# Performance work log

Measured on AMD Instinct MI355X. Metric: run time of the kernel, lower is better.

Reference implementation:

```python
import jax, jax.numpy as jnp
import numpy as np

N_GRID = 262144   # grid vertices (all local, empty halo)
N_MESH = 40962    # icosahedral mesh level-6 vertices
N_EDGES = 524288  # mesh2grid bipartite edges
H = 128           # cfg.model.hidden_dim
LN_EPS = 1e-5


def layer_norm(x, g, b):
    m = jnp.mean(x, axis=-1, keepdims=True)
    v = jnp.var(x, axis=-1, keepdims=True)
    return (x - m) * jax.lax.rsqrt(v + LN_EPS) * g + b


def setup_inputs() -> dict:
    key = jax.random.key(0)
    ks = jax.random.split(key, 12)
    def w(k, shape, fan_in):
        return jax.random.normal(k, shape, jnp.float32) * (fan_in ** -0.5)
    return {
        "mesh2grid_edge_features": jax.random.normal(ks[0], (N_EDGES, H), jnp.float32),
        "grid_node_features": jax.random.normal(ks[1], (N_GRID, H), jnp.float32),
        "mesh_node_features": jax.random.normal(ks[2], (N_MESH, H), jnp.float32),
        # edge MLP: Linear(3H->H) -> SiLU -> Linear(H->H) -> LayerNorm, residual
        "edge_W1": w(ks[3], (3 * H, H), 3 * H), "edge_b1": jnp.zeros((H,), jnp.float32),
        "edge_W2": w(ks[4], (H, H), H), "edge_b2": jnp.zeros((H,), jnp.float32),
        "edge_ln_g": jnp.ones((H,), jnp.float32), "edge_ln_b": jnp.zeros((H,), jnp.float32),
        # node MLP: Linear(2H->H) -> SiLU -> Linear(H->H) -> LayerNorm
        "node_W1": w(ks[5], (2 * H, H), 2 * H), "node_b1": jnp.zeros((H,), jnp.float32),
        "node_W2": w(ks[6], (H, H), H), "node_b2": jnp.zeros((H,), jnp.float32),
        "node_ln_g": jnp.ones((H,), jnp.float32), "node_ln_b": jnp.zeros((H,), jnp.float32),
        "src_indices": jax.random.randint(ks[7], (N_EDGES,), 0, N_MESH, jnp.int32),
        "dst_indices": jax.random.randint(ks[8], (N_EDGES,), 0, N_GRID, jnp.int32),
    }


def reference(mesh2grid_edge_features, grid_node_features, mesh_node_features,
              edge_W1, edge_b1, edge_W2, edge_b2, edge_ln_g, edge_ln_b,
              node_W1, node_b1, node_W2, node_b2, node_ln_g, node_ln_b,
              src_indices, dst_indices):
    # --- edge block: gather src (mesh) / dst (grid), MLP, LN, residual ---
    src = mesh_node_features[src_indices]        # [E, H]  (augmented mesh == mesh, empty halo)
    dst = grid_node_features[dst_indices]        # [E, H]
    xe = jnp.concatenate([src, dst, mesh2grid_edge_features], axis=-1)  # [E, 3H]
    he = (jax.nn.silu(xe @ edge_W1 + edge_b1)) @ edge_W2 + edge_b2
    e_feats = mesh2grid_edge_features + layer_norm(he, edge_ln_g, edge_ln_b)  # [E, H]
    # --- node block: scatter-sum edges to grid nodes, MLP, LN ---
    agg = jax.ops.segment_sum(e_feats, dst_indices, num_segments=N_GRID)  # [N_grid, H]
    xn = jnp.concatenate([grid_node_features, agg], axis=-1)              # [N_grid, 2H]
    hn = (jax.nn.silu(xn @ node_W1 + node_b1)) @ node_W2 + node_b2
    n_feats = layer_norm(hn, node_ln_g, node_ln_b)
    return grid_node_features + n_feats
```

## Files before the change

### kernel.cpp

```cpp
#include <hip/hip_runtime.h>
#include <stdint.h>

#define HDIM 128
#define NGRID 262144
#define NMESH 40962
#define NEDGE 524288

typedef __attribute__((ext_vector_type(8))) short short8;
typedef __attribute__((ext_vector_type(4))) float f32x4;

__device__ __forceinline__ unsigned short f2bf(float f) {
  union { float f; uint32_t u; } v; v.f = f;
  uint32_t u = v.u;
  u += 0x7fffu + ((u >> 16) & 1u);
  return (unsigned short)(u >> 16);
}
__device__ __forceinline__ float bf2f(unsigned short h) {
  union { uint32_t u; float f; } v; v.u = ((uint32_t)h) << 16;
  return v.f;
}
__device__ __forceinline__ short8 cvt8(float4 a, float4 b) {
  short8 r;
  r[0] = (short)f2bf(a.x); r[1] = (short)f2bf(a.y);
  r[2] = (short)f2bf(a.z); r[3] = (short)f2bf(a.w);
  r[4] = (short)f2bf(b.x); r[5] = (short)f2bf(b.y);
  r[6] = (short)f2bf(b.z); r[7] = (short)f2bf(b.w);
  return r;
}

__global__ void pack_weights(const float* __restrict__ eW1, const float* __restrict__ eW2,
                             const float* __restrict__ nW1, const float* __restrict__ nW2,
                             unsigned short* __restrict__ ws)
{
  int i = blockIdx.x * 256 + threadIdx.x;
  unsigned short* eW1T = ws;
  unsigned short* eW2T = ws + 49152;
  unsigned short* nW1T = ws + 65536;
  unsigned short* nW2T = ws + 98304;
  if (i < 49152) {
    int c = i / 384, k = i % 384;
    eW1T[i] = f2bf(eW1[(size_t)k * 128 + c]);
  } else if (i < 65536) {
    int j = i - 49152; int c = j / 128, k = j % 128;
    eW2T[j] = f2bf(eW2[(size_t)k * 128 + c]);
  } else if (i < 98304) {
    int j = i - 65536; int c = j / 256, k = j % 256;
    nW1T[j] = f2bf(nW1[(size_t)k * 128 + c]);
  } else if (i < 114688) {
    int j = i - 98304; int c = j / 128, k = j % 128;
    nW2T[j] = f2bf(nW2[(size_t)k * 128 + c]);
  }
}

__global__ __launch_bounds__(256, 4)
void edge_kernel(const float* __restrict__ ef, const float* __restrict__ gridf,
                 const float* __restrict__ mesh,
                 const unsigned short* __restrict__ W1T, const unsigned short* __restrict__ W2T,
                 const float* __restrict__ b1, const float* __restrict__ b2,
                 const float* __restrict__ lng, const float* __restrict__ lnb,
                 const int* __restrict__ src, const int* __restrict__ dst,
                 float* __restrict__ agg)
{
  __shared__ __align__(16) unsigned short h1s[64][136];

  const int tid  = threadIdx.x;
  const int wave = tid >> 6;
  const int lane = tid & 63;
  const int l16  = lane & 15;
  const int g4   = lane >> 4;
  const int e0   = blockIdx.x * 64;
  const int arow = wave * 16 + l16;

  const int myS = src[e0 + arow];
  const int myD = dst[e0 + arow];
  const float* rowS = mesh  + (size_t)myS * HDIM;
  const float* rowD = gridf + (size_t)myD * HDIM;
  const float* rowE = ef    + (size_t)(e0 + arow) * HDIM;

  f32x4 acc[8];
  #pragma unroll
  for (int c = 0; c < 8; ++c) acc[c] = (f32x4){0.f, 0.f, 0.f, 0.f};

  const unsigned short* wl1 = W1T + (size_t)l16 * 384 + g4 * 8;

  #pragma unroll
  for (int part = 0; part < 3; ++part) {
    const float* base = (part == 0) ? rowS : (part == 1) ? rowD : rowE;
    #pragma unroll
    for (int kk = 0; kk < 4; ++kk) {
      const int ks = part * 4 + kk;
      const float* ap = base + kk * 32 + g4 * 8;
      float4 f0 = *reinterpret_cast<const float4*>(ap);
      float4 f1 = *reinterpret_cast<const float4*>(ap + 4);
      short8 a = cvt8(f0, f1);
      #pragma unroll
      for (int c = 0; c < 8; ++c) {
        short8 b = *reinterpret_cast<const short8*>(wl1 + (size_t)c * 16 * 384 + ks * 32);
        acc[c] = __builtin_amdgcn_mfma_f32_16x16x32_bf16(a, b, acc[c], 0, 0, 0);
      }
    }
  }

  #pragma unroll
  for (int c = 0; c < 8; ++c) {
    const int col = c * 16 + l16;
    float bb = b1[col];
    #pragma unroll
    for (int r = 0; r < 4; ++r) {
      float x = acc[c][r] + bb;
      float s = x / (1.f + __expf(-x));
      unsigned int h = f2bf(s);
      unsigned int other = __shfl_xor((int)h, 1);
      unsigned int packed = (l16 & 1) ? ((h << 16) | other) : ((other << 16) | h);
      if ((l16 & 1) == (r & 1)) {
        *reinterpret_cast<unsigned int*>(&h1s[wave * 16 + g4 * 4 + r][c * 16 + (l16 & ~1)]) = packed;
      }
    }
  }
  __syncthreads();

  f32x4 acc2[8];
  #pragma unroll
  for (int c = 0; c < 8; ++c) acc2[c] = (f32x4){0.f, 0.f, 0.f, 0.f};

  const unsigned short* wl2 = W2T + (size_t)l16 * 128 + g4 * 8;
  #pragma unroll
  for (int ks = 0; ks < 4; ++ks) {
    short8 a = *reinterpret_cast<const short8*>(&h1s[arow][ks * 32 + g4 * 8]);
    #pragma unroll
    for (int c = 0; c < 8; ++c) {
      short8 b = *reinterpret_cast<const short8*>(wl2 + (size_t)c * 16 * 128 + ks * 32);
      acc2[c] = __builtin_amdgcn_mfma_f32_16x16x32_bf16(a, b, acc2[c], 0, 0, 0);
    }
  }

  float vs[4] = {0.f, 0.f, 0.f, 0.f};
  float vq[4] = {0.f, 0.f, 0.f, 0.f};
  #pragma unroll
  for (int c = 0; c < 8; ++c) {
    float bb = b2[c * 16 + l16];
    #pragma unroll
    for (int r = 0; r < 4; ++r) {
      float x = acc2[c][r] + bb;
      acc2[c][r] = x;
      vs[r] += x;
      vq[r] += x * x;
    }
  }
  #pragma unroll
  for (int m = 1; m < 16; m <<= 1) {
    #pragma unroll
    for (int r = 0; r < 4; ++r) {
      vs[r] += __shfl_xor(vs[r], m);
      vq[r] += __shfl_xor(vq[r], m);
    }
  }
  float mean[4], rstd[4];
  #pragma unroll
  for (int r = 0; r < 4; ++r) {
    mean[r] = vs[r] * (1.f / 128.f);
    float var = vq[r] * (1.f / 128.f) - mean[r] * mean[r];
    rstd[r] = rsqrtf(var + 1e-5f);
  }
  int drow[4];
  #pragma unroll
  for (int r = 0; r < 4; ++r) drow[r] = dst[e0 + wave * 16 + g4 * 4 + r];

  #pragma unroll
  for (int c = 0; c < 8; ++c) {
    const int col = c * 16 + l16;
    float gg = lng[col], bb = lnb[col];
    #pragma unroll
    for (int r = 0; r < 4; ++r) {
      const int row = wave * 16 + g4 * 4 + r;
      float y = (acc2[c][r] - mean[r]) * rstd[r] * gg + bb;
      float e = ef[(size_t)(e0 + row) * HDIM + col] + y;
      unsafeAtomicAdd(&agg[(size_t)drow[r] * HDIM + col], e);
    }
  }
}

__global__ __launch_bounds__(256, 4)
void node_kernel(const float* __restrict__ gridf,
                 const unsigned short* __restrict__ W1T, const unsigned short* __restrict__ W2T,
                 const float* __restrict__ b1, const float* __restrict__ b2,
                 const float* __restrict__ lng, const float* __restrict__ lnb,
                 float* __restrict__ out)
{
  __shared__ __align__(16) unsigned short h1s[64][136];

  const int tid  = threadIdx.x;
  const int wave = tid >> 6;
  const int lane = tid & 63;
  const int l16  = lane & 15;
  const int g4   = lane >> 4;
  const int n0   = blockIdx.x * 64;
  const int arow = wave * 16 + l16;

  const float* rowG = gridf + (size_t)(n0 + arow) * HDIM;
  const float* rowA = out   + (size_t)(n0 + arow) * HDIM;

  f32x4 acc[8];
  #pragma unroll
  for (int c = 0; c < 8; ++c) acc[c] = (f32x4){0.f, 0.f, 0.f, 0.f};

  const unsigned short* wl1 = W1T + (size_t)l16 * 256 + g4 * 8;

  #pragma unroll
  for (int part = 0; part < 2; ++part) {
    const float* base = (part == 0) ? rowG : rowA;
    #pragma unroll
    for (int kk = 0; kk < 4; ++kk) {
      const int ks = part * 4 + kk;
      const float* ap = base + kk * 32 + g4 * 8;
      float4 f0 = *reinterpret_cast<const float4*>(ap);
      float4 f1 = *reinterpret_cast<const float4*>(ap + 4);
      short8 a = cvt8(f0, f1);
      #pragma unroll
      for (int c = 0; c < 8; ++c) {
        short8 b = *reinterpret_cast<const short8*>(wl1 + (size_t)c * 16 * 256 + ks * 32);
        acc[c] = __builtin_amdgcn_mfma_f32_16x16x32_bf16(a, b, acc[c], 0, 0, 0);
      }
    }
  }

  #pragma unroll
  for (int c = 0; c < 8; ++c) {
    const int col = c * 16 + l16;
    float bb = b1[col];
    #pragma unroll
    for (int r = 0; r < 4; ++r) {
      float x = acc[c][r] + bb;
      float s = x / (1.f + __expf(-x));
      unsigned int h = f2bf(s);
      unsigned int other = __shfl_xor((int)h, 1);
      unsigned int packed = (l16 & 1) ? ((h << 16) | other) : ((other << 16) | h);
      if ((l16 & 1) == (r & 1)) {
        *reinterpret_cast<unsigned int*>(&h1s[wave * 16 + g4 * 4 + r][c * 16 + (l16 & ~1)]) = packed;
      }
    }
  }
  __syncthreads();

  f32x4 acc2[8];
  #pragma unroll
  for (int c = 0; c < 8; ++c) acc2[c] = (f32x4){0.f, 0.f, 0.f, 0.f};

  const unsigned short* wl2 = W2T + (size_t)l16 * 128 + g4 * 8;
  #pragma unroll
  for (int ks = 0; ks < 4; ++ks) {
    short8 a = *reinterpret_cast<const short8*>(&h1s[arow][ks * 32 + g4 * 8]);
    #pragma unroll
    for (int c = 0; c < 8; ++c) {
      short8 b = *reinterpret_cast<const short8*>(wl2 + (size_t)c * 16 * 128 + ks * 32);
      acc2[c] = __builtin_amdgcn_mfma_f32_16x16x32_bf16(a, b, acc2[c], 0, 0, 0);
    }
  }

  float vs[4] = {0.f, 0.f, 0.f, 0.f};
  float vq[4] = {0.f, 0.f, 0.f, 0.f};
  #pragma unroll
  for (int c = 0; c < 8; ++c) {
    float bb = b2[c * 16 + l16];
    #pragma unroll
    for (int r = 0; r < 4; ++r) {
      float x = acc2[c][r] + bb;
      acc2[c][r] = x;
      vs[r] += x;
      vq[r] += x * x;
    }
  }
  #pragma unroll
  for (int m = 1; m < 16; m <<= 1) {
    #pragma unroll
    for (int r = 0; r < 4; ++r) {
      vs[r] += __shfl_xor(vs[r], m);
      vq[r] += __shfl_xor(vq[r], m);
    }
  }
  float mean[4], rstd[4];
  #pragma unroll
  for (int r = 0; r < 4; ++r) {
    mean[r] = vs[r] * (1.f / 128.f);
    float var = vq[r] * (1.f / 128.f) - mean[r] * mean[r];
    rstd[r] = rsqrtf(var + 1e-5f);
  }
  #pragma unroll
  for (int c = 0; c < 8; ++c) {
    const int col = c * 16 + l16;
    float gg = lng[col], bb = lnb[col];
    #pragma unroll
    for (int r = 0; r < 4; ++r) {
      const int row = wave * 16 + g4 * 4 + r;
      size_t idx = (size_t)(n0 + row) * HDIM + col;
      float y = (acc2[c][r] - mean[r]) * rstd[r] * gg + bb;
      out[idx] = gridf[idx] + y;
    }
  }
}

extern "C" void kernel_launch(void* const* d_in, const int* in_sizes, int n_in,
                              void* d_out, int out_size, void* d_ws, size_t ws_size,
                              hipStream_t stream)
{
  (void)in_sizes; (void)n_in; (void)out_size; (void)ws_size;
  const float* ef   = (const float*)d_in[0];
  const float* grid = (const float*)d_in[1];
  const float* mesh = (const float*)d_in[2];
  const float* eW1  = (const float*)d_in[3];
  const float* eb1  = (const float*)d_in[4];
  const float* eW2  = (const float*)d_in[5];
  const float* eb2  = (const float*)d_in[6];
  const float* elng = (const float*)d_in[7];
  const float* elnb = (const float*)d_in[8];
  const float* nW1  = (const float*)d_in[9];
  const float* nb1  = (const float*)d_in[10];
  const float* nW2  = (const float*)d_in[11];
  const float* nb2  = (const float*)d_in[12];
  const float* nlng = (const float*)d_in[13];
  const float* nlnb = (const float*)d_in[14];
  const int* src    = (const int*)d_in[15];
  const int* dst    = (const int*)d_in[16];
  float* out = (float*)d_out;
  unsigned short* ws = (unsigned short*)d_ws;

  hipMemsetAsync(out, 0, (size_t)NGRID * HDIM * sizeof(float), stream);
  pack_weights<<<448, 256, 0, stream>>>(eW1, eW2, nW1, nW2, ws);
  edge_kernel<<<NEDGE / 64, 256, 0, stream>>>(ef, grid, mesh,
      ws, ws + 49152, eb1, eb2, elng, elnb, src, dst, out);
  node_kernel<<<NGRID / 64, 256, 0, stream>>>(grid,
      ws + 65536, ws + 98304, nb1, nb2, nlng, nlnb, out);
}
```

Measured before the change: 957.4 us.

## Sort edges by destination and replace atomic scatter with CSR segmented reduce

Adds a counting sort of edges by destination: histogram, three-pass scan and scatter, with packed src/dst/edge ids. When the workspace is large enough, the edge kernel processes edges in sorted order and writes per-edge bf16 results. The node kernel then sums each grid node's contiguous edge range through row pointers, which removes the float atomics and the output memset. The change also drops the block barrier between the two matmuls, since each wave reads back only its own rows. In exchange it adds several preprocessing launches, a large bf16 intermediate buffer and some precision loss from storing edge outputs in bf16.

```diff
diff --git a/kernel.cpp b/kernel.cpp
--- a/kernel.cpp
+++ b/kernel.cpp
@@ -8,96 +8,158 @@
 
 typedef __attribute__((ext_vector_type(8))) short short8;
 typedef __attribute__((ext_vector_type(4))) float f32x4;
-
-__device__ __forceinline__ unsigned short f2bf(float f) {
-  union { float f; uint32_t u; } v; v.f = f;
-  uint32_t u = v.u;
+typedef unsigned int u32;
+typedef unsigned long long u64;
+
+#define WS_COUNT   0x000000u
+#define WS_ROWPTR  0x100000u
+#define WS_WLOC    0x200010u
+#define WS_BSUM    0x300100u
+#define WS_SORTED  0x310000u
+#define WS_WEIGHTS 0x800000u
+#define WS_ESORT   0x840000u
+#define WE1 0u
+#define WE2 49152u
+#define WN1 65536u
+#define WN2 98304u
+
+static __device__ __forceinline__ u32 f2bf_u(float f) {
+  union { float f; u32 u; } v; v.f = f;
+  u32 u = v.u;
   u += 0x7fffu + ((u >> 16) & 1u);
-  return (unsigned short)(u >> 16);
-}
-__device__ __forceinline__ float bf2f(unsigned short h) {
-  union { uint32_t u; float f; } v; v.u = ((uint32_t)h) << 16;
+  return u >> 16;
+}
+static __device__ __forceinline__ unsigned short f2bf(float f) { return (unsigned short)f2bf_u(f); }
+static __device__ __forceinline__ float bf2f(unsigned short h) {
+  union { u32 u; float f; } v; v.u = ((u32)h) << 16;
   return v.f;
 }
-__device__ __forceinline__ short8 cvt8(float4 a, float4 b) {
+static __device__ __forceinline__ short8 cvt8(const float* p) {
+  float4 f0 = *(const float4*)p;
+  float4 f1 = *(const float4*)(p + 4);
   short8 r;
-  r[0] = (short)f2bf(a.x); r[1] = (short)f2bf(a.y);
-  r[2] = (short)f2bf(a.z); r[3] = (short)f2bf(a.w);
-  r[4] = (short)f2bf(b.x); r[5] = (short)f2bf(b.y);
-  r[6] = (short)f2bf(b.z); r[7] = (short)f2bf(b.w);
+  r[0] = (short)f2bf_u(f0.x); r[1] = (short)f2bf_u(f0.y);
+  r[2] = (short)f2bf_u(f0.z); r[3] = (short)f2bf_u(f0.w);
+  r[4] = (short)f2bf_u(f1.x); r[5] = (short)f2bf_u(f1.y);
+  r[6] = (short)f2bf_u(f1.z); r[7] = (short)f2bf_u(f1.w);
   return r;
 }
 
 __global__ void pack_weights(const float* __restrict__ eW1, const float* __restrict__ eW2,
                              const float* __restrict__ nW1, const float* __restrict__ nW2,
-                             unsigned short* __restrict__ ws)
+                             unsigned short* __restrict__ wp)
 {
   int i = blockIdx.x * 256 + threadIdx.x;
-  unsigned short* eW1T = ws;
-  unsigned short* eW2T = ws + 49152;
-  unsigned short* nW1T = ws + 65536;
-  unsigned short* nW2T = ws + 98304;
   if (i < 49152) {
     int c = i / 384, k = i % 384;
-    eW1T[i] = f2bf(eW1[(size_t)k * 128 + c]);
+    wp[WE1 + i] = f2bf(eW1[(size_t)k * 128 + c]);
   } else if (i < 65536) {
     int j = i - 49152; int c = j / 128, k = j % 128;
-    eW2T[j] = f2bf(eW2[(size_t)k * 128 + c]);
+    wp[WE2 + j] = f2bf(eW2[(size_t)k * 128 + c]);
   } else if (i < 98304) {
     int j = i - 65536; int c = j / 256, k = j % 256;
-    nW1T[j] = f2bf(nW1[(size_t)k * 128 + c]);
+    wp[WN1 + j] = f2bf(nW1[(size_t)k * 128 + c]);
   } else if (i < 114688) {
     int j = i - 98304; int c = j / 128, k = j % 128;
-    nW2T[j] = f2bf(nW2[(size_t)k * 128 + c]);
-  }
-}
-
+    wp[WN2 + j] = f2bf(nW2[(size_t)k * 128 + c]);
+  }
+}
+
+__global__ void hist_k(const int* __restrict__ dst, u32* __restrict__ cnt) {
+  int e = blockIdx.x * 256 + threadIdx.x;
+  atomicAdd(&cnt[dst[e]], 1u);
+}
+
+__global__ void scan1(const u32* __restrict__ cnt, u32* __restrict__ rp, u32* __restrict__ bsum) {
+  int t = threadIdx.x, b = blockIdx.x;
+  int i0 = b * 1024 + t * 4;
+  uint4 v = *(const uint4*)(cnt + i0);
+  u32 s = v.x + v.y + v.z + v.w;
+  u32 sc = s;
+  #pragma unroll
+  for (int d = 1; d < 64; d <<= 1) {
+    u32 n = (u32)__shfl_up((int)sc, d);
+    if ((t & 63) >= d) sc += n;
+  }
+  __shared__ u32 wsum[4];
+  if ((t & 63) == 63) wsum[t >> 6] = sc;
+  __syncthreads();
+  u32 woff = 0;
+  for (int w = 0; w < (t >> 6); ++w) woff += wsum[w];
+  u32 ex = woff + sc - s;
+  rp[i0] = ex; rp[i0 + 1] = ex + v.x; rp[i0 + 2] = ex + v.x + v.y; rp[i0 + 3] = ex + v.x + v.y + v.z;
+  if (t == 255) bsum[b] = woff + sc;
+}
+
+__global__ void scan2(u32* __restrict__ bsum) {
+  int t = threadIdx.x;
+  u32 s = bsum[t];
+  u32 sc = s;
+  #pragma unroll
+  for (int d = 1; d < 64; d <<= 1) {
+    u32 n = (u32)__shfl_up((int)sc, d);
+    if ((t & 63) >= d) sc += n;
+  }
+  __shared__ u32 wsum[4];
+  if ((t & 63) == 63) wsum[t >> 6] = sc;
+  __syncthreads();
+  u32 woff = 0;
+  for (int w = 0; w < (t >> 6); ++w) woff += wsum[w];
+  bsum[t] = woff + sc - s;
+}
+
+__global__ void scan3(u32* __restrict__ rp, u32* __restrict__ wloc, const u32* __restrict__ bsum) {
+  int t = threadIdx.x, b = blockIdx.x;
+  int i0 = b * 1024 + t * 4;
+  u32 off = bsum[b];
+  #pragma unroll
+  for (int j = 0; j < 4; ++j) { u32 vv = rp[i0 + j] + off; rp[i0 + j] = vv; wloc[i0 + j] = vv; }
+  if (b == 0 && t == 0) rp[NGRID] = NEDGE;
+}
+
+__global__ void scatter_k(const int* __restrict__ src, const int* __restrict__ dst,
+                          u32* __restrict__ wloc, u64* __restrict__ sorted) {
+  int e = blockIdx.x * 256 + threadIdx.x;
+  int d = dst[e];
+  u32 pos = atomicAdd(&wloc[d], 1u);
+  sorted[pos] = (u64)(u32)src[e] | ((u64)(u32)d << 16) | ((u64)(u32)e << 34);
+}
+
+template<bool SORTEDOUT>
 __global__ __launch_bounds__(256, 4)
 void edge_kernel(const float* __restrict__ ef, const float* __restrict__ gridf,
-                 const float* __restrict__ mesh,
-                 const unsigned short* __restrict__ W1T, const unsigned short* __restrict__ W2T,
+                 const float* __restrict__ mesh, const unsigned short* __restrict__ wp,
                  const float* __restrict__ b1, const float* __restrict__ b2,
                  const float* __restrict__ lng, const float* __restrict__ lnb,
-                 const int* __restrict__ src, const int* __restrict__ dst,
-                 float* __restrict__ agg)
+                 const u64* __restrict__ sorted,
+                 unsigned short* __restrict__ esort, float* __restrict__ aggf)
 {
   __shared__ __align__(16) unsigned short h1s[64][136];
 
   const int tid  = threadIdx.x;
-  const int wave = tid >> 6;
-  const int lane = tid & 63;
-  const int l16  = lane & 15;
-  const int g4   = lane >> 4;
+  const int wave = tid >> 6, lane = tid & 63, l16 = lane & 15, g4 = lane >> 4;
   const int e0   = blockIdx.x * 64;
   const int arow = wave * 16 + l16;
 
-  const int myS = src[e0 + arow];
-  const int myD = dst[e0 + arow];
-  const float* rowS = mesh  + (size_t)myS * HDIM;
-  const float* rowD = gridf + (size_t)myD * HDIM;
-  const float* rowE = ef    + (size_t)(e0 + arow) * HDIM;
+  const u64 sv = sorted[e0 + arow];
+  const float* rowS = mesh  + (size_t)(sv & 0xffffu) * HDIM;
+  const float* rowD = gridf + (size_t)((sv >> 16) & 0x3ffffu) * HDIM;
+  const float* rowE = ef    + (size_t)(sv >> 34) * HDIM;
+
+  const unsigned short* wl1 = wp + WE1 + (size_t)l16 * 384 + g4 * 8;
+  const unsigned short* wl2 = wp + WE2 + (size_t)l16 * 128 + g4 * 8;
 
   f32x4 acc[8];
   #pragma unroll
   for (int c = 0; c < 8; ++c) acc[c] = (f32x4){0.f, 0.f, 0.f, 0.f};
-
-  const unsigned short* wl1 = W1T + (size_t)l16 * 384 + g4 * 8;
-
-  #pragma unroll
-  for (int part = 0; part < 3; ++part) {
-    const float* base = (part == 0) ? rowS : (part == 1) ? rowD : rowE;
-    #pragma unroll
-    for (int kk = 0; kk < 4; ++kk) {
-      const int ks = part * 4 + kk;
-      const float* ap = base + kk * 32 + g4 * 8;
-      float4 f0 = *reinterpret_cast<const float4*>(ap);
-      float4 f1 = *reinterpret_cast<const float4*>(ap + 4);
-      short8 a = cvt8(f0, f1);
-      #pragma unroll
-      for (int c = 0; c < 8; ++c) {
-        short8 b = *reinterpret_cast<const short8*>(wl1 + (size_t)c * 16 * 384 + ks * 32);
-        acc[c] = __builtin_amdgcn_mfma_f32_16x16x32_bf16(a, b, acc[c], 0, 0, 0);
-      }
+  #pragma unroll
+  for (int ks = 0; ks < 12; ++ks) {
+    const float* base = (ks < 4) ? rowS : (ks < 8) ? rowD : rowE;
+    short8 a = cvt8(base + (ks & 3) * 32 + g4 * 8);
+    #pragma unroll
+    for (int c = 0; c < 8; ++c) {
+      short8 b = *(const short8*)(wl1 + (size_t)c * 16 * 384 + ks * 32);
+      acc[c] = __builtin_amdgcn_mfma_f32_16x16x32_bf16(a, b, acc[c], 0, 0, 0);
     }
   }
 
@@ -109,27 +171,24 @@
     for (int r = 0; r < 4; ++r) {
       float x = acc[c][r] + bb;
       float s = x / (1.f + __expf(-x));
-      unsigned int h = f2bf(s);
-      unsigned int other = __shfl_xor((int)h, 1);
-      unsigned int packed = (l16 & 1) ? ((h << 16) | other) : ((other << 16) | h);
+      unsigned h = f2bf_u(s);
+      unsigned other = (unsigned)__shfl_xor((int)h, 1);
+      unsigned packed = (l16 & 1) ? ((h << 16) | other) : ((other << 16) | h);
       if ((l16 & 1) == (r & 1)) {
-        *reinterpret_cast<unsigned int*>(&h1s[wave * 16 + g4 * 4 + r][c * 16 + (l16 & ~1)]) = packed;
+        *(u32*)(&h1s[wave * 16 + g4 * 4 + r][col & ~1]) = packed;
       }
     }
   }
-  __syncthreads();
 
   f32x4 acc2[8];
   #pragma unroll
   for (int c = 0; c < 8; ++c) acc2[c] = (f32x4){0.f, 0.f, 0.f, 0.f};
-
-  const unsigned short* wl2 = W2T + (size_t)l16 * 128 + g4 * 8;
   #pragma unroll
   for (int ks = 0; ks < 4; ++ks) {
-    short8 a = *reinterpret_cast<const short8*>(&h1s[arow][ks * 32 + g4 * 8]);
+    short8 a = *(const short8*)(&h1s[arow][ks * 32 + g4 * 8]);
     #pragma unroll
     for (int c = 0; c < 8; ++c) {
-      short8 b = *reinterpret_cast<const short8*>(wl2 + (size_t)c * 16 * 128 + ks * 32);
+      short8 b = *(const short8*)(wl2 + (size_t)c * 16 * 128 + ks * 32);
       acc2[c] = __builtin_amdgcn_mfma_f32_16x16x32_bf16(a, b, acc2[c], 0, 0, 0);
     }
   }
@@ -143,8 +202,7 @@
     for (int r = 0; r < 4; ++r) {
       float x = acc2[c][r] + bb;
       acc2[c][r] = x;
-      vs[r] += x;
-      vq[r] += x * x;
+      vs[r] += x; vq[r] += x * x;
     }
   }
   #pragma unroll
@@ -162,9 +220,10 @@
     float var = vq[r] * (1.f / 128.f) - mean[r] * mean[r];
     rstd[r] = rsqrtf(var + 1e-5f);
   }
-  int drow[4];
-  #pragma unroll
-  for (int r = 0; r < 4; ++r) drow[r] = dst[e0 + wave * 16 + g4 * 4 + r];
+
+  u64 svr[4];
+  #pragma unroll
+  for (int r = 0; r < 4; ++r) svr[r] = (u64)__shfl((long long)sv, g4 * 4 + r);
 
   #pragma unroll
   for (int c = 0; c < 8; ++c) {
@@ -173,54 +232,94 @@
     #pragma unroll
     for (int r = 0; r < 4; ++r) {
       const int row = wave * 16 + g4 * 4 + r;
-      float y = (acc2[c][r] - mean[r]) * rstd[r] * gg + bb;
-      float e = ef[(size_t)(e0 + row) * HDIM + col] + y;
-      unsafeAtomicAdd(&agg[(size_t)drow[r] * HDIM + col], e);
-    }
-  }
-}
-
-__global__ __launch_bounds__(256, 4)
-void node_kernel(const float* __restrict__ gridf,
-                 const unsigned short* __restrict__ W1T, const unsigned short* __restrict__ W2T,
+      float y = (acc2[c][r] - mean[r]) * rstd[r] * gg + bb
+              + ef[(size_t)(svr[r] >> 34) * HDIM + col];
+      if (SORTEDOUT) {
+        unsigned h = f2bf_u(y);
+        unsigned other = (unsigned)__shfl_xor((int)h, 1);
+        unsigned packed = (l16 & 1) ? ((h << 16) | other) : ((other << 16) | h);
+        if ((l16 & 1) == (r & 1)) {
+          *(u32*)(&h1s[row][col & ~1]) = packed;
+        }
+      } else {
+        unsafeAtomicAdd(&aggf[(size_t)((svr[r] >> 16) & 0x3ffffu) * HDIM + col], y);
+      }
+    }
+  }
+
+  if (SORTEDOUT) {
+    __syncthreads();
+    const int row = tid >> 2, ch = tid & 3;
+    uint4* d = (uint4*)(esort + (size_t)(e0 + row) * HDIM + ch * 32);
+    const uint4* s = (const uint4*)(&h1s[row][ch * 32]);
+    d[0] = s[0]; d[1] = s[1]; d[2] = s[2]; d[3] = s[3];
+  }
+}
+
+template<bool FROMWS>
+__global__ __launch_bounds__(256, 3)
+void node_kernel(const float* __restrict__ gridf, const unsigned short* __restrict__ wp,
                  const float* __restrict__ b1, const float* __restrict__ b2,
                  const float* __restrict__ lng, const float* __restrict__ lnb,
-                 float* __restrict__ out)
+                 const u32* __restrict__ rowptr, const unsigned short* __restrict__ esort,
+                 const float* __restrict__ aggf, float* __restrict__ out)
 {
   __shared__ __align__(16) unsigned short h1s[64][136];
 
   const int tid  = threadIdx.x;
-  const int wave = tid >> 6;
-  const int lane = tid & 63;
-  const int l16  = lane & 15;
-  const int g4   = lane >> 4;
+  const int wave = tid >> 6, lane = tid & 63, l16 = lane & 15, g4 = lane >> 4;
   const int n0   = blockIdx.x * 64;
   const int arow = wave * 16 + l16;
-
-  const float* rowG = gridf + (size_t)(n0 + arow) * HDIM;
-  const float* rowA = out   + (size_t)(n0 + arow) * HDIM;
+  const int n    = n0 + arow;
+  const float* rowG = gridf + (size_t)n * HDIM;
+
+  float sm[4][8];
+  #pragma unroll
+  for (int kk = 0; kk < 4; ++kk)
+    #pragma unroll
+    for (int i = 0; i < 8; ++i) sm[kk][i] = 0.f;
+
+  if (FROMWS) {
+    const u32 rs = rowptr[n], re = rowptr[n + 1];
+    for (u32 p = rs; p < re; ++p) {
+      const unsigned short* rp8 = esort + (size_t)p * HDIM + g4 * 8;
+      #pragma unroll
+      for (int kk = 0; kk < 4; ++kk) {
+        short8 v = *(const short8*)(rp8 + kk * 32);
+        #pragma unroll
+        for (int i = 0; i < 8; ++i) sm[kk][i] += bf2f((unsigned short)v[i]);
+      }
+    }
+  } else {
+    #pragma unroll
+    for (int kk = 0; kk < 4; ++kk) {
+      const float* ap = aggf + (size_t)n * HDIM + kk * 32 + g4 * 8;
+      #pragma unroll
+      for (int i = 0; i < 8; ++i) sm[kk][i] = ap[i];
+    }
+  }
+
+  const unsigned short* wl1 = wp + WN1 + (size_t)l16 * 256 + g4 * 8;
+  const unsigned short* wl2 = wp + WN2 + (size_t)l16 * 128 + g4 * 8;
 
   f32x4 acc[8];
   #pragma unroll
   for (int c = 0; c < 8; ++c) acc[c] = (f32x4){0.f, 0.f, 0.f, 0.f};
-
-  const unsigned short* wl1 = W1T + (size_t)l16 * 256 + g4 * 8;
-
-  #pragma unroll
-  for (int part = 0; part < 2; ++part) {
-    const float* base = (part == 0) ? rowG : rowA;
-    #pragma unroll
-    for (int kk = 0; kk < 4; ++kk) {
-      const int ks = part * 4 + kk;
-      const float* ap = base + kk * 32 + g4 * 8;
-      float4 f0 = *reinterpret_cast<const float4*>(ap);
-      float4 f1 = *reinterpret_cast<const float4*>(ap + 4);
-      short8 a = cvt8(f0, f1);
+  #pragma unroll
+  for (int ks = 0; ks < 8; ++ks) {
+    short8 a;
+    if (ks < 4) {
+      a = cvt8(rowG + ks * 32 + g4 * 8);
+    } else {
+      short8 t;
       #pragma unroll
-      for (int c = 0; c < 8; ++c) {
-        short8 b = *reinterpret_cast<const short8*>(wl1 + (size_t)c * 16 * 256 + ks * 32);
-        acc[c] = __builtin_amdgcn_mfma_f32_16x16x32_bf16(a, b, acc[c], 0, 0, 0);
-      }
+      for (int i = 0; i < 8; ++i) t[i] = (short)f2bf_u(sm[ks - 4][i]);
+      a = t;
+    }
+    #pragma unroll
+    for (int c = 0; c < 8; ++c) {
+      short8 b = *(const short8*)(wl1 + (size_t)c * 16 * 256 + ks * 32);
+      acc[c] = __builtin_amdgcn_mfma_f32_16x16x32_bf16(a, b, acc[c], 0, 0, 0);
     }
   }
 
@@ -232,27 +331,24 @@
     for (int r = 0; r < 4; ++r) {
       float x = acc[c][r] + bb;
       float s = x / (1.f + __expf(-x));
-      unsigned int h = f2bf(s);
-      unsigned int other = __shfl_xor((int)h, 1);
-      unsigned int packed = (l16 & 1) ? ((h << 16) | other) : ((other << 16) | h);
+      unsigned h = f2bf_u(s);
+      unsigned other = (unsigned)__shfl_xor((int)h, 1);
+      unsigned packed = (l16 & 1) ? ((h << 16) | other) : ((other << 16) | h);
       if ((l16 & 1) == (r & 1)) {
-        *reinterpret_cast<unsigned int*>(&h1s[wave * 16 + g4 * 4 + r][c * 16 + (l16 & ~1)]) = packed;
+        *(u32*)(&h1s[wave * 16 + g4 * 4 + r][col & ~1]) = packed;
       }
     }
   }
-  __syncthreads();
 
   f32x4 acc2[8];
   #pragma unroll
   for (int c = 0; c < 8; ++c) acc2[c] = (f32x4){0.f, 0.f, 0.f, 0.f};
-
-  const unsigned short* wl2 = W2T + (size_t)l16 * 128 + g4 * 8;
   #pragma unroll
   for (int ks = 0; ks < 4; ++ks) {
-    short8 a = *reinterpret_cast<const short8*>(&h1s[arow][ks * 32 + g4 * 8]);
+    short8 a = *(const short8*)(&h1s[arow][ks * 32 + g4 * 8]);
     #pragma unroll
     for (int c = 0; c < 8; ++c) {
-      short8 b = *reinterpret_cast<const short8*>(wl2 + (size_t)c * 16 * 128 + ks * 32);
+      short8 b = *(const short8*)(wl2 + (size_t)c * 16 * 128 + ks * 32);
       acc2[c] = __builtin_amdgcn_mfma_f32_16x16x32_bf16(a, b, acc2[c], 0, 0, 0);
     }
   }
@@ -266,8 +362,7 @@
     for (int r = 0; r < 4; ++r) {
       float x = acc2[c][r] + bb;
       acc2[c][r] = x;
-      vs[r] += x;
-      vq[r] += x * x;
+      vs[r] += x; vq[r] += x * x;
     }
   }
   #pragma unroll
@@ -303,7 +398,7 @@
                               void* d_out, int out_size, void* d_ws, size_t ws_size,
                               hipStream_t stream)
 {
-  (void)in_sizes; (void)n_in; (void)out_size; (void)ws_size;
+  (void)in_sizes; (void)n_in; (void)out_size;
   const float* ef   = (const float*)d_in[0];
   const float* grid = (const float*)d_in[1];
   const float* mesh = (const float*)d_in[2];
@@ -322,12 +417,37 @@
   const int* src    = (const int*)d_in[15];
   const int* dst    = (const int*)d_in[16];
   float* out = (float*)d_out;
-  unsigned short* ws = (unsigned short*)d_ws;
-
-  hipMemsetAsync(out, 0, (size_t)NGRID * HDIM * sizeof(float), stream);
-  pack_weights<<<448, 256, 0, stream>>>(eW1, eW2, nW1, nW2, ws);
-  edge_kernel<<<NEDGE / 64, 256, 0, stream>>>(ef, grid, mesh,
-      ws, ws + 49152, eb1, eb2, elng, elnb, src, dst, out);
-  node_kernel<<<NGRID / 64, 256, 0, stream>>>(grid,
-      ws + 65536, ws + 98304, nb1, nb2, nlng, nlnb, out);
-}
+
+  unsigned char* wsb = (unsigned char*)d_ws;
+  u32* cnt  = (u32*)(wsb + WS_COUNT);
+  u32* rp   = (u32*)(wsb + WS_ROWPTR);
+  u32* wloc = (u32*)(wsb + WS_WLOC);
+  u32* bsum = (u32*)(wsb + WS_BSUM);
+  u64* sorted = (u64*)(wsb + WS_SORTED);
+  unsigned short* wp = (unsigned short*)(wsb + WS_WEIGHTS);
+  unsigned short* esort = (unsigned short*)(wsb + WS_ESORT);
+
+  const size_t REQUIRED = (size_t)WS_ESORT + (size_t)NEDGE * HDIM * 2;
+  const bool fast = ws_size >= REQUIRED;
+
+  hipMemsetAsync(cnt, 0, (size_t)NGRID * 4, stream);
+  pack_weights<<<448, 256, 0, stream>>>(eW1, eW2, nW1, nW2, wp);
+  hist_k<<<NEDGE / 256, 256, 0, stream>>>(dst, cnt);
+  scan1<<<256, 256, 0, stream>>>(cnt, rp, bsum);
+  scan2<<<1, 256, 0, stream>>>(bsum);
+  scan3<<<256, 256, 0, stream>>>(rp, wloc, bsum);
+  scatter_k<<<NEDGE / 256, 256, 0, stream>>>(src, dst, wloc, sorted);
+
+  if (fast) {
+    edge_kernel<true><<<NEDGE / 64, 256, 0, stream>>>(ef, grid, mesh, wp,
+        eb1, eb2, elng, elnb, sorted, esort, nullptr);
+    node_kernel<true><<<NGRID / 64, 256, 0, stream>>>(grid, wp,
+        nb1, nb2, nlng, nlnb, rp, esort, nullptr, out);
+  } else {
+    hipMemsetAsync(out, 0, (size_t)NGRID * HDIM * sizeof(float), stream);
+    edge_kernel<false><<<NEDGE / 64, 256, 0, stream>>>(ef, grid, mesh, wp,
+        eb1, eb2, elng, elnb, sorted, nullptr, out);
+    node_kernel<false><<<NGRID / 64, 256, 0, stream>>>(grid, wp,
+        nb1, nb2, nlng, nlnb, rp, nullptr, out, out);
+  }
+}
```

Measured after the change: 926.1 us. 1.03x faster.
